# Kernel tuning notes

Measured on AMD Instinct MI355X. Metric: run time of the kernel, lower is better.

## Reference

```python
import jax, jax.numpy as jnp
import numpy as np
import math

B, L = 16, 100
NC = 80
STRIDES = (8.0, 16.0, 32.0)
ANCHORS = np.array([[10., 13.], [16., 30.], [33., 23.], [30., 61.], [62., 45.],
                    [59., 119.], [116., 90.], [156., 198.], [373., 326.]], np.float32)
ANCH_MASKS = ((0, 1, 2), (3, 4, 5), (6, 7, 8))
THRESH = 4.0          # gt_match_max_ratio
CIOU_RATIO = 1.0
W_BOX, W_OBJ, W_CLS = 0.05, 1.0, 0.58
OV = 0.5              # overlap in assign_targets_to_proposals


def _bce(x, z):
    # binary_cross_entropy_with_logits, elementwise
    return -(z * jax.nn.log_sigmoid(x) + (1.0 - z) * jax.nn.log_sigmoid(-x))


def _ciou_xywh(b1, b2, eps=1e-9):
    # b1, b2: [M,4] center-x, center-y, w, h  (matches _bbox_iou with x1y1x2y2=False, CIoU=True)
    b1x1, b1x2 = b1[:, 0] - b1[:, 2] / 2, b1[:, 0] + b1[:, 2] / 2
    b1y1, b1y2 = b1[:, 1] - b1[:, 3] / 2, b1[:, 1] + b1[:, 3] / 2
    b2x1, b2x2 = b2[:, 0] - b2[:, 2] / 2, b2[:, 0] + b2[:, 2] / 2
    b2y1, b2y2 = b2[:, 1] - b2[:, 3] / 2, b2[:, 1] + b2[:, 3] / 2
    inter = jnp.clip(jnp.minimum(b1x2, b2x2) - jnp.maximum(b1x1, b2x1), 0) * \
            jnp.clip(jnp.minimum(b1y2, b2y2) - jnp.maximum(b1y1, b2y1), 0)
    w1, h1 = b1x2 - b1x1, b1y2 - b1y1 + eps
    w2, h2 = b2x2 - b2x1, b2y2 - b2y1 + eps
    union = w1 * h1 + w2 * h2 - inter + eps
    iou = inter / union
    cw = jnp.maximum(b1x2, b2x2) - jnp.minimum(b1x1, b2x1)
    ch = jnp.maximum(b1y2, b2y2) - jnp.minimum(b1y1, b2y1)
    c2 = cw ** 2 + ch ** 2 + eps
    rho2 = ((b2x1 + b2x2 - b1x1 - b1x2) ** 2 + (b2y1 + b2y2 - b1y1 - b1y2) ** 2) / 4
    v = (4.0 / math.pi ** 2) * (jnp.arctan(w2 / h2) - jnp.arctan(w1 / h1)) ** 2
    alpha = jax.lax.stop_gradient(v / (1.0 + eps - iou + v))  # torch.no_grad()
    return iou - (rho2 / c2 + v * alpha)


def _yolo_loss(y_pred0, y_pred1, y_pred2, y_true):
    # valid GT rows: nlabel counts rows with positive sum; valid rows assumed contiguous at front
    nlabel = (y_true.sum(-1) > 0).sum(-1)                                # [B]
    valid = (jnp.arange(L)[None, :] < nlabel[:, None]).reshape(-1)       # [N]
    batch_ids = jnp.repeat(jnp.arange(B), L)                             # [N]
    flat = y_true.reshape(-1, 5)
    gt_labels = flat[:, 4].astype(jnp.int32)
    # convert x1,y1,w,h -> cx,cy,w,h
    gt_boxes = jnp.concatenate([flat[:, :2] + flat[:, 2:4] / 2, flat[:, 2:4]], axis=1)
    N = B * L
    offsets = jnp.array([[0, 0], [-OV, 0], [0, -OV], [OV, 0], [0, OV]], jnp.float32)
    loss_box = jnp.float32(0.0)
    loss_obj = jnp.float32(0.0)
    loss_cls = jnp.float32(0.0)
    for li, out in enumerate((y_pred0, y_pred1, y_pred2)):
        s = STRIDES[li]
        anch = jnp.asarray(ANCHORS[list(ANCH_MASKS[li])] / s)            # [3,2] grid units
        H, Wd = out.shape[2], out.shape[3]
        nch = 5 + NC
        p = out.reshape(B, -1, nch, H, Wd).transpose(0, 1, 3, 4, 2)      # [B,3,H,W,nch]
        sgb = gt_boxes / s                                               # [N,4]
        # size_matched_idx
        r = sgb[:, None, 2:4] / anch[None]                               # [N,3,2]
        maxr = jnp.maximum(r, 1.0 / r).max(-1)                           # [N,3]
        match = (maxr < THRESH) & valid[:, None]                         # [N,3]
        # assign_targets_to_proposals: 5 offset candidates per (gt, anchor)
        x, y = sgb[:, 0], sgb[:, 1]
        fx, fy = jnp.mod(x, 1.0), jnp.mod(y, 1.0)
        cond = jnp.stack([
            jnp.ones_like(x, bool),
            (x > 1) & (fx < OV),
            (y > 1) & (fy < OV),
            (x < Wd - 1) & (fx > 1 - OV),
            (y < H - 1) & (fy > 1 - OV),
        ], axis=1)                                                       # [N,5]
        coords = (sgb[:, None, :2] + offsets[None]).astype(jnp.int32)    # [N,5,2] (trunc like .long())
        cmask = (match[:, :, None] & cond[:, None, :]).reshape(-1)       # [N*3*5]
        bf = jnp.broadcast_to(batch_ids[:, None, None], (N, 3, 5)).reshape(-1)
        af = jnp.broadcast_to(jnp.arange(3)[None, :, None], (N, 3, 5)).reshape(-1)
        gf = jnp.broadcast_to(jnp.arange(N)[:, None, None], (N, 3, 5)).reshape(-1)
        gxy = jnp.broadcast_to(coords[:, None, :, :], (N, 3, 5, 2)).reshape(-1, 2)
        gx, gy = gxy[:, 0], gxy[:, 1]
        pred = p[bf, af, gy, gx]                                         # [M,nch] (OOB gathers clamped; masked out)
        pxy = jax.nn.sigmoid(pred[:, :2]) + gxy.astype(pred.dtype)
        pwh = jnp.exp(pred[:, 2:4]) * anch[af]
        pbox = jnp.concatenate([pxy, pwh], axis=1)
        ci = _ciou_xywh(pbox, sgb[gf])                                   # [M]
        cm = cmask.astype(pred.dtype)
        nval = cm.sum()
        denom = jnp.maximum(nval, 1.0)
        loss_box = loss_box + jnp.where(nval > 0, ((1.0 - ci) * cm).sum() / denom, 0.0)
        # objectness target scatter (invalid candidates dropped via OOB batch index)
        obj_val = CIOU_RATIO * jnp.clip(ci, 0) + (1.0 - CIOU_RATIO)
        bs = jnp.where(cmask, bf, B)
        gt_obj = jnp.zeros((B, 3, H, Wd), pred.dtype).at[bs, af, gy, gx].set(obj_val, mode='drop')
        if NC > 1:
            zhot = jax.nn.one_hot(gt_labels[gf], NC, dtype=pred.dtype)
            bce_c = _bce(pred[:, 5:], zhot)
            loss_cls = loss_cls + jnp.where(nval > 0, (bce_c * cm[:, None]).sum() / (denom * NC), 0.0)
        loss_obj = loss_obj + _bce(p[..., 4], gt_obj).mean()
    lb, lo, lc = W_BOX * loss_box, W_OBJ * loss_obj, W_CLS * loss_cls
    return lb + lo + lc, lb, lo, lc


def setup_inputs():
    rng = np.random.default_rng(0)
    k0, k1, k2 = jax.random.split(jax.random.key(0), 3)
    y_pred0 = jax.random.normal(k0, (B, 3 * (5 + NC), 80, 80), jnp.float32)
    y_pred1 = jax.random.normal(k1, (B, 3 * (5 + NC), 40, 40), jnp.float32)
    y_pred2 = jax.random.normal(k2, (B, 3 * (5 + NC), 20, 20), jnp.float32)
    yt = np.zeros((B, L, 5), np.float32)
    n_valid = 70  # valid labels contiguous at the front, rest zero-padded
    yt[:, :n_valid, 0] = rng.uniform(1.0, 560.0, (B, n_valid))
    yt[:, :n_valid, 1] = rng.uniform(1.0, 560.0, (B, n_valid))
    yt[:, :n_valid, 2] = rng.uniform(8.0, 80.0, (B, n_valid))
    yt[:, :n_valid, 3] = rng.uniform(8.0, 80.0, (B, n_valid))
    yt[:, :n_valid, 4] = rng.integers(0, NC, (B, n_valid)).astype(np.float32)
    return {"y_pred0": y_pred0, "y_pred1": y_pred1, "y_pred2": y_pred2, "y_true": jnp.asarray(yt)}


def reference(y_pred0, y_pred1, y_pred2, y_true):
    return _yolo_loss(y_pred0, y_pred1, y_pred2, y_true)
```

## Files before the change

### kernel.cpp

```cpp
#include <hip/hip_runtime.h>
#include <math.h>

#define BB 16
#define LL 100
#define NCLS 80
#define CPB 282
#define CAP 288
#define NBLK 256
#define NTHR 1024

__device__ __constant__ int   d_W[3]     = {80, 40, 20};
__device__ __constant__ int   d_HW[3]    = {6400, 1600, 400};
__device__ __constant__ float d_stride[3]= {8.f, 16.f, 32.f};
__device__ __constant__ int   d_gtoff[3] = {0, 307200, 384000};
__device__ __constant__ float d_anch[3][3][2] = {
  {{10.f,13.f},{16.f,30.f},{33.f,23.f}},
  {{30.f,61.f},{62.f,45.f},{59.f,119.f}},
  {{116.f,90.f},{156.f,198.f},{373.f,326.f}}};


__device__ __forceinline__ float softplusf(float t) {
  return fmaxf(t, 0.f) + log1pf(expf(-fabsf(t)));
}
__device__ __forceinline__ float sigmoidf_(float x) {
  return 1.f / (1.f + expf(-x));
}

__device__ __forceinline__ float ciou_(float px, float py, float pw, float ph,
                                       float gx, float gy, float gw, float gh) {
  const float eps = 1e-9f;
  float b1x1 = px - pw*0.5f, b1x2 = px + pw*0.5f;
  float b1y1 = py - ph*0.5f, b1y2 = py + ph*0.5f;
  float b2x1 = gx - gw*0.5f, b2x2 = gx + gw*0.5f;
  float b2y1 = gy - gh*0.5f, b2y2 = gy + gh*0.5f;
  float iw = fmaxf(fminf(b1x2,b2x2) - fmaxf(b1x1,b2x1), 0.f);
  float ih = fmaxf(fminf(b1y2,b2y2) - fmaxf(b1y1,b2y1), 0.f);
  float inter = iw*ih;
  float w1 = b1x2-b1x1, h1 = b1y2-b1y1 + eps;
  float w2 = b2x2-b2x1, h2 = b2y2-b2y1 + eps;
  float uni = w1*h1 + w2*h2 - inter + eps;
  float iou = inter/uni;
  float cw = fmaxf(b1x2,b2x2) - fminf(b1x1,b2x1);
  float ch = fmaxf(b1y2,b2y2) - fminf(b1y1,b2y1);
  float c2 = cw*cw + ch*ch + eps;
  float dx = b2x1+b2x2-b1x1-b1x2;
  float dy = b2y1+b2y2-b1y1-b1y2;
  float rho2 = (dx*dx + dy*dy)*0.25f;
  float at = atanf(w2/h2) - atanf(w1/h1);
  float v = (float)(4.0/(M_PI*M_PI)) * at*at;
  float alpha = v / (1.0f + eps - iou + v);
  return iou - (rho2/c2 + v*alpha);
}

__global__ __launch_bounds__(NTHR)
void k_main(const float* __restrict__ p0, const float* __restrict__ p1,
            const float* __restrict__ p2, const float* __restrict__ yt,
            float* __restrict__ acc, float* __restrict__ out)
{
  __shared__ int s_nl[2];
  __shared__ int s_cnt;
  __shared__ unsigned s_cand[CAP];
  __shared__ float s_acc[15];

  const int blk = blockIdx.x, tid = threadIdx.x;

  if (tid < 2)  s_nl[tid] = 0;
  if (tid == 2) s_cnt = 0;
  if (tid >= 4 && tid < 19) s_acc[tid-4] = 0.f;

  const int t0 = blk*CPB;
  const int b_lo = t0/4500;
  int b_hi = (t0 + CPB - 1)/4500; if (b_hi > BB-1) b_hi = BB-1;
  __syncthreads();

  if (tid < LL) {
    const float* row = yt + (size_t)(b_lo*LL + tid)*5;
    if (row[0]+row[1]+row[2]+row[3]+row[4] > 0.f) atomicAdd(&s_nl[0], 1);
  } else if (tid >= 128 && tid < 128+LL && b_hi != b_lo) {
    const float* row = yt + (size_t)(b_hi*LL + (tid-128))*5;
    if (row[0]+row[1]+row[2]+row[3]+row[4] > 0.f) atomicAdd(&s_nl[1], 1);
  }
  __syncthreads();

  if (tid < CPB) {
    int t = t0 + tid;
    if (t < BB*LL*45) {
      int b = t/4500; int rem = t - b*4500;
      int g_loc = rem/45; int rem2 = rem - g_loc*45;
      int lvl = rem2/15, ao = rem2 - lvl*15, a = ao/5, o = ao - a*5;
      const float* row = yt + (size_t)(b*LL + g_loc)*5;
      float s = d_stride[lvl];
      int W = d_W[lvl];
      float cx = (row[0] + row[2]*0.5f)/s;
      float cy = (row[1] + row[3]*0.5f)/s;
      float w = row[2]/s, h = row[3]/s;
      float aw = d_anch[lvl][a][0]/s, ah = d_anch[lvl][a][1]/s;
      float rw = w/aw, rh = h/ah;
      float maxr = fmaxf(fmaxf(rw,1.f/rw), fmaxf(rh,1.f/rh));
      int nl = (b == b_lo) ? s_nl[0] : s_nl[1];
      bool m = (g_loc < nl) && (maxr < 4.0f);
      float fx = cx - floorf(cx), fy = cy - floorf(cy);
      bool c;
      switch (o) {
        case 0: c = true; break;
        case 1: c = (cx > 1.f) && (fx < 0.5f); break;
        case 2: c = (cy > 1.f) && (fy < 0.5f); break;
        case 3: c = (cx < (float)(W-1)) && (fx > 0.5f); break;
        default:c = (cy < (float)(W-1)) && (fy > 0.5f); break;
      }
      if (m && c) {
        const float offx[5] = {0.f,-0.5f,0.f,0.5f,0.f};
        const float offy[5] = {0.f,0.f,-0.5f,0.f,0.5f};
        int gx = (int)(cx + offx[o]);
        int gy = (int)(cy + offy[o]);
        int g = b*LL + g_loc;
        unsigned pk = ((unsigned)lvl<<27) | ((unsigned)a<<25) | ((unsigned)g<<14)
                    | ((unsigned)gy<<7) | (unsigned)gx;
        int idx = atomicAdd(&s_cnt, 1);
        s_cand[idx] = pk;
      }
    }
  }

  {
    int gt = blk*NTHR + tid;
    if (gt < 100800) {
      int e0 = gt*4;
      int lvl = (e0 < 307200) ? 0 : (e0 < 384000 ? 1 : 2);
      int HW = d_HW[lvl];
      int idx = e0 - d_gtoff[lvl];
      int b = idx/(3*HW); int r2 = idx - b*3*HW; int a = r2/HW; int pos = r2 - a*HW;
      const float* pr = (lvl==0) ? p0 : (lvl==1) ? p1 : p2;
      const float4 x4 = *(const float4*)(pr + (size_t)((b*255 + a*85 + 4)*HW + pos));
      float sp = softplusf(x4.x) + softplusf(x4.y) + softplusf(x4.z) + softplusf(x4.w);
      atomicAdd(&s_acc[9+lvl], sp);
    }
  }
  __syncthreads();

  {
    int wave = tid >> 6, lane = tid & 63;
    int n = s_cnt;
    float a0=0,a1=0,a2=0, c0=0,c1=0,c2=0, n0=0,n1=0,n2=0, z0=0,z1=0,z2=0;
    for (int i = wave; i < n; i += 16) {
      unsigned pk = s_cand[i];
      int gx  = pk & 127;
      int gy  = (pk>>7) & 127;
      int g   = (pk>>14) & 2047;
      int a   = (pk>>25) & 3;
      int lvl = (pk>>27) & 3;
      int b = g / LL;
      float s = d_stride[lvl];
      int W = d_W[lvl], HW = d_HW[lvl];
      const float* pr = (lvl==0) ? p0 : (lvl==1) ? p1 : p2;
      const float* row = yt + (size_t)g*5;
      float cx = (row[0] + row[2]*0.5f)/s;
      float cy = (row[1] + row[3]*0.5f)/s;
      float w  = row[2]/s, h = row[3]/s;
      int label = (int)row[4];
      float aw = d_anch[lvl][a][0]/s, ah = d_anch[lvl][a][1]/s;

      const float* base = pr + (size_t)((b*255 + a*85)*HW + gy*W + gx);
      float xA = base[(size_t)lane*HW];
      float xB = (lane < 21) ? base[(size_t)(64+lane)*HW] : 0.f;
      float x0 = __shfl(xA,0), x1 = __shfl(xA,1), x2 = __shfl(xA,2), x3 = __shfl(xA,3);
      float xobj = __shfl(xA,4);

      float pxc = sigmoidf_(x0) + (float)gx;
      float pyc = sigmoidf_(x1) + (float)gy;
      float pw = expf(x2)*aw, ph = expf(x3)*ah;
      float ci = ciou_(pxc,pyc,pw,ph, cx,cy,w,h);

      float cls = 0.f;
      if (lane >= 5) { int cc = lane-5;  cls += (cc==label) ? softplusf(-xA) : softplusf(xA); }
      if (lane < 21) { int cc = 59+lane; cls += (cc==label) ? softplusf(-xB) : softplusf(xB); }
      for (int off = 1; off < 64; off <<= 1) cls += __shfl_xor(cls, off);

      float bx = 1.f - ci;
      float zx = fmaxf(ci, 0.f) * xobj;
      if      (lvl == 0) { a0 += bx; c0 += cls; n0 += 1.f; z0 += zx; }
      else if (lvl == 1) { a1 += bx; c1 += cls; n1 += 1.f; z1 += zx; }
      else               { a2 += bx; c2 += cls; n2 += 1.f; z2 += zx; }
    }
    if (lane == 0) {
      if (n0 != 0.f) { atomicAdd(&s_acc[0],a0); atomicAdd(&s_acc[3],c0);
                       atomicAdd(&s_acc[6],n0); atomicAdd(&s_acc[12],z0); }
      if (n1 != 0.f) { atomicAdd(&s_acc[1],a1); atomicAdd(&s_acc[4],c1);
                       atomicAdd(&s_acc[7],n1); atomicAdd(&s_acc[13],z1); }
      if (n2 != 0.f) { atomicAdd(&s_acc[2],a2); atomicAdd(&s_acc[5],c2);
                       atomicAdd(&s_acc[8],n2); atomicAdd(&s_acc[14],z2); }
    }
  }
  __syncthreads();
  if (tid < 15 && s_acc[tid] != 0.f) atomicAdd(&acc[tid], s_acc[tid]);
  __syncthreads();

  if (tid == 0) {
    __threadfence();
    unsigned old = atomicAdd((unsigned int*)&acc[15], 1u);
    if (old == (unsigned)(gridDim.x - 1)) {
      float A[15];
      #pragma unroll
      for (int k = 0; k < 15; ++k) A[k] = atomicAdd(&acc[k], 0.0f);
      const float cells[3] = {307200.f, 76800.f, 19200.f};
      float lb = 0.f, lc = 0.f, lo = 0.f;
      for (int l = 0; l < 3; ++l) {
        float nval  = A[6+l];
        float denom = fmaxf(nval, 1.f);
        if (nval > 0.f) {
          lb += A[l] / denom;
          lc += A[3+l] / (denom * (float)NCLS);
        }
        lo += (A[9+l] - A[12+l]) / cells[l];
      }
      lb *= 0.05f;
      lc *= 0.58f;
      out[0] = lb + lo + lc;
      out[1] = lb;
      out[2] = lo;
      out[3] = lc;
    }
  }
}

extern "C" void kernel_launch(void* const* d_in, const int* in_sizes, int n_in,
                              void* d_out, int out_size, void* d_ws, size_t ws_size,
                              hipStream_t stream) {
  const float* p0 = (const float*)d_in[0];
  const float* p1 = (const float*)d_in[1];
  const float* p2 = (const float*)d_in[2];
  const float* yt = (const float*)d_in[3];
  float* acc = (float*)d_ws;

  hipMemsetAsync(acc, 0, 16*sizeof(float), stream);
  k_main<<<NBLK, NTHR, 0, stream>>>(p0, p1, p2, yt, acc, (float*)d_out);
}
```

Before: 55.47 us.

## Split fused loss kernel into prep, wide gather, and finalize kernels

Splits the single fused kernel into three launches. Candidate generation writes its packed candidates to global workspace, and a second kernel assigns one wave per candidate slot across 4608 blocks plus 99 blocks for the objectness softplus sum. A tiny final kernel replaces the last-block atomic-counter finalization and the memset. The aim is to spread the serial per-block candidate loop across far more waves, at the cost of two extra launches and many blocks that find no candidate in their slot.

```diff
diff --git a/kernel.cpp b/kernel.cpp
--- a/kernel.cpp
+++ b/kernel.cpp
@@ -6,7 +6,9 @@
 #define NCLS 80
 #define CPB 282
 #define CAP 288
-#define NBLK 256
+#define PREPB 256
+#define GATB 4608
+#define OBJB 99
 #define NTHR 1024
 
 __device__ __constant__ int   d_W[3]     = {80, 40, 20};
@@ -18,6 +20,9 @@
   {{30.f,61.f},{62.f,45.f},{59.f,119.f}},
   {{116.f,90.f},{156.f,198.f},{373.f,326.f}}};
 
+#define ACC_OFF   0
+#define CNT_OFF   16
+#define CANDG_OFF 272
 
 __device__ __forceinline__ float softplusf(float t) {
   return fmaxf(t, 0.f) + log1pf(expf(-fabsf(t)));
@@ -52,21 +57,18 @@
   return iou - (rho2/c2 + v*alpha);
 }
 
-__global__ __launch_bounds__(NTHR)
-void k_main(const float* __restrict__ p0, const float* __restrict__ p1,
-            const float* __restrict__ p2, const float* __restrict__ yt,
-            float* __restrict__ acc, float* __restrict__ out)
+__global__ __launch_bounds__(512)
+void k_prep(const float* __restrict__ yt, float* __restrict__ acc,
+            unsigned int* __restrict__ cntg, unsigned int* __restrict__ candg)
 {
   __shared__ int s_nl[2];
   __shared__ int s_cnt;
-  __shared__ unsigned s_cand[CAP];
-  __shared__ float s_acc[15];
-
   const int blk = blockIdx.x, tid = threadIdx.x;
+
+  if (blk == 0 && tid >= 32 && tid < 48) acc[tid-32] = 0.f;
 
   if (tid < 2)  s_nl[tid] = 0;
   if (tid == 2) s_cnt = 0;
-  if (tid >= 4 && tid < 19) s_acc[tid-4] = 0.f;
 
   const int t0 = blk*CPB;
   const int b_lo = t0/4500;
@@ -117,33 +119,33 @@
         unsigned pk = ((unsigned)lvl<<27) | ((unsigned)a<<25) | ((unsigned)g<<14)
                     | ((unsigned)gy<<7) | (unsigned)gx;
         int idx = atomicAdd(&s_cnt, 1);
-        s_cand[idx] = pk;
+        candg[blk*CAP + idx] = pk;
       }
     }
   }
-
-  {
-    int gt = blk*NTHR + tid;
-    if (gt < 100800) {
-      int e0 = gt*4;
-      int lvl = (e0 < 307200) ? 0 : (e0 < 384000 ? 1 : 2);
-      int HW = d_HW[lvl];
-      int idx = e0 - d_gtoff[lvl];
-      int b = idx/(3*HW); int r2 = idx - b*3*HW; int a = r2/HW; int pos = r2 - a*HW;
-      const float* pr = (lvl==0) ? p0 : (lvl==1) ? p1 : p2;
-      const float4 x4 = *(const float4*)(pr + (size_t)((b*255 + a*85 + 4)*HW + pos));
-      float sp = softplusf(x4.x) + softplusf(x4.y) + softplusf(x4.z) + softplusf(x4.w);
-      atomicAdd(&s_acc[9+lvl], sp);
-    }
-  }
-  __syncthreads();
-
-  {
-    int wave = tid >> 6, lane = tid & 63;
-    int n = s_cnt;
-    float a0=0,a1=0,a2=0, c0=0,c1=0,c2=0, n0=0,n1=0,n2=0, z0=0,z1=0,z2=0;
-    for (int i = wave; i < n; i += 16) {
-      unsigned pk = s_cand[i];
+  __syncthreads();
+  if (tid == 0) cntg[blk] = (unsigned)s_cnt;
+}
+
+__global__ __launch_bounds__(NTHR)
+void k_gather(const float* __restrict__ p0, const float* __restrict__ p1,
+              const float* __restrict__ p2, const float* __restrict__ yt,
+              const unsigned int* __restrict__ cntg,
+              const unsigned int* __restrict__ candg,
+              float* __restrict__ acc)
+{
+  __shared__ float s_acc[15];
+  const int blk = blockIdx.x, tid = threadIdx.x;
+  if (tid < 15) s_acc[tid] = 0.f;
+  __syncthreads();
+
+  if (blk < GATB) {
+    int wg = blk*16 + (tid >> 6);
+    int lane = tid & 63;
+    int p = wg / CAP;
+    int sIdx = wg - p*CAP;
+    if (sIdx < (int)cntg[p]) {
+      unsigned pk = candg[p*CAP + sIdx];
       int gx  = pk & 127;
       int gy  = (pk>>7) & 127;
       int g   = (pk>>14) & 2047;
@@ -176,51 +178,53 @@
       if (lane < 21) { int cc = 59+lane; cls += (cc==label) ? softplusf(-xB) : softplusf(xB); }
       for (int off = 1; off < 64; off <<= 1) cls += __shfl_xor(cls, off);
 
-      float bx = 1.f - ci;
-      float zx = fmaxf(ci, 0.f) * xobj;
-      if      (lvl == 0) { a0 += bx; c0 += cls; n0 += 1.f; z0 += zx; }
-      else if (lvl == 1) { a1 += bx; c1 += cls; n1 += 1.f; z1 += zx; }
-      else               { a2 += bx; c2 += cls; n2 += 1.f; z2 += zx; }
-    }
-    if (lane == 0) {
-      if (n0 != 0.f) { atomicAdd(&s_acc[0],a0); atomicAdd(&s_acc[3],c0);
-                       atomicAdd(&s_acc[6],n0); atomicAdd(&s_acc[12],z0); }
-      if (n1 != 0.f) { atomicAdd(&s_acc[1],a1); atomicAdd(&s_acc[4],c1);
-                       atomicAdd(&s_acc[7],n1); atomicAdd(&s_acc[13],z1); }
-      if (n2 != 0.f) { atomicAdd(&s_acc[2],a2); atomicAdd(&s_acc[5],c2);
-                       atomicAdd(&s_acc[8],n2); atomicAdd(&s_acc[14],z2); }
+      if (lane == 0) {
+        float bx = 1.f - ci;
+        float zx = fmaxf(ci, 0.f) * xobj;
+        atomicAdd(&s_acc[lvl],     bx);
+        atomicAdd(&s_acc[3+lvl],  cls);
+        atomicAdd(&s_acc[6+lvl],  1.f);
+        atomicAdd(&s_acc[12+lvl], zx);
+      }
+    }
+  } else {
+    int gt = (blk - GATB)*NTHR + tid;
+    if (gt < 100800) {
+      int e0 = gt*4;
+      int lvl = (e0 < 307200) ? 0 : (e0 < 384000 ? 1 : 2);
+      int HW = d_HW[lvl];
+      int idx = e0 - d_gtoff[lvl];
+      int b = idx/(3*HW); int r2 = idx - b*3*HW; int a = r2/HW; int pos = r2 - a*HW;
+      const float* pr = (lvl==0) ? p0 : (lvl==1) ? p1 : p2;
+      const float4 x4 = *(const float4*)(pr + (size_t)((b*255 + a*85 + 4)*HW + pos));
+      float sp = softplusf(x4.x) + softplusf(x4.y) + softplusf(x4.z) + softplusf(x4.w);
+      atomicAdd(&s_acc[9+lvl], sp);
     }
   }
   __syncthreads();
   if (tid < 15 && s_acc[tid] != 0.f) atomicAdd(&acc[tid], s_acc[tid]);
-  __syncthreads();
-
-  if (tid == 0) {
-    __threadfence();
-    unsigned old = atomicAdd((unsigned int*)&acc[15], 1u);
-    if (old == (unsigned)(gridDim.x - 1)) {
-      float A[15];
-      #pragma unroll
-      for (int k = 0; k < 15; ++k) A[k] = atomicAdd(&acc[k], 0.0f);
-      const float cells[3] = {307200.f, 76800.f, 19200.f};
-      float lb = 0.f, lc = 0.f, lo = 0.f;
-      for (int l = 0; l < 3; ++l) {
-        float nval  = A[6+l];
-        float denom = fmaxf(nval, 1.f);
-        if (nval > 0.f) {
-          lb += A[l] / denom;
-          lc += A[3+l] / (denom * (float)NCLS);
-        }
-        lo += (A[9+l] - A[12+l]) / cells[l];
-      }
-      lb *= 0.05f;
-      lc *= 0.58f;
-      out[0] = lb + lo + lc;
-      out[1] = lb;
-      out[2] = lo;
-      out[3] = lc;
-    }
-  }
+}
+
+__global__ __launch_bounds__(64)
+void k_fin(const float* __restrict__ acc, float* __restrict__ out) {
+  if (threadIdx.x != 0) return;
+  const float cells[3] = {307200.f, 76800.f, 19200.f};
+  float lb = 0.f, lc = 0.f, lo = 0.f;
+  for (int l = 0; l < 3; ++l) {
+    float nval  = acc[6+l];
+    float denom = fmaxf(nval, 1.f);
+    if (nval > 0.f) {
+      lb += acc[l] / denom;
+      lc += acc[3+l] / (denom * (float)NCLS);
+    }
+    lo += (acc[9+l] - acc[12+l]) / cells[l];
+  }
+  lb *= 0.05f;
+  lc *= 0.58f;
+  out[0] = lb + lo + lc;
+  out[1] = lb;
+  out[2] = lo;
+  out[3] = lc;
 }
 
 extern "C" void kernel_launch(void* const* d_in, const int* in_sizes, int n_in,
@@ -230,8 +234,13 @@
   const float* p1 = (const float*)d_in[1];
   const float* p2 = (const float*)d_in[2];
   const float* yt = (const float*)d_in[3];
-  float* acc = (float*)d_ws;
-
-  hipMemsetAsync(acc, 0, 16*sizeof(float), stream);
-  k_main<<<NBLK, NTHR, 0, stream>>>(p0, p1, p2, yt, acc, (float*)d_out);
-}
+
+  float*        wsf   = (float*)d_ws;
+  float*        acc   = wsf + ACC_OFF;
+  unsigned int* cntg  = (unsigned int*)(wsf + CNT_OFF);
+  unsigned int* candg = (unsigned int*)(wsf + CANDG_OFF);
+
+  k_prep  <<<PREPB, 512, 0, stream>>>(yt, acc, cntg, candg);
+  k_gather<<<GATB + OBJB, NTHR, 0, stream>>>(p0, p1, p2, yt, cntg, candg, acc);
+  k_fin   <<<1, 64, 0, stream>>>(acc, (float*)d_out);
+}
```

Result: faster. 47.71 us (-14.0%).

## Split loss kernel into prep, compaction and wide gather stages

Applied to the files above, without the earlier changes.

The single fused kernel is split into three launches. The first builds candidate matches per block into global memory. A single-block prefix scan then compacts them into one list. A wide gather kernel spreads candidates across many more waves, roughly one per wave, while dedicated blocks handle the objectness softplus sum. The aim is to remove the long serial per-block candidate loop, at the cost of two extra launches and a serial copy loop in the compaction kernel.

```diff
diff --git a/kernel.cpp b/kernel.cpp
--- a/kernel.cpp
+++ b/kernel.cpp
@@ -6,7 +6,9 @@
 #define NCLS 80
 #define CPB 282
 #define CAP 288
-#define NBLK 256
+#define PREPB 256
+#define OBJB 99
+#define GATB 1024
 #define NTHR 1024
 
 __device__ __constant__ int   d_W[3]     = {80, 40, 20};
@@ -18,6 +20,11 @@
   {{30.f,61.f},{62.f,45.f},{59.f,119.f}},
   {{116.f,90.f},{156.f,198.f},{373.f,326.f}}};
 
+#define ACC_OFF    0
+#define CNT_OFF    16
+#define CANDG_OFF  272
+#define PACK_OFF   74000
+#define NCAND_OFF  146000
 
 __device__ __forceinline__ float softplusf(float t) {
   return fmaxf(t, 0.f) + log1pf(expf(-fabsf(t)));
@@ -52,21 +59,18 @@
   return iou - (rho2/c2 + v*alpha);
 }
 
-__global__ __launch_bounds__(NTHR)
-void k_main(const float* __restrict__ p0, const float* __restrict__ p1,
-            const float* __restrict__ p2, const float* __restrict__ yt,
-            float* __restrict__ acc, float* __restrict__ out)
+__global__ __launch_bounds__(512)
+void k_prep(const float* __restrict__ yt, float* __restrict__ acc,
+            unsigned int* __restrict__ cntg, unsigned int* __restrict__ candg)
 {
   __shared__ int s_nl[2];
   __shared__ int s_cnt;
-  __shared__ unsigned s_cand[CAP];
-  __shared__ float s_acc[15];
-
   const int blk = blockIdx.x, tid = threadIdx.x;
+
+  if (blk == 0 && tid >= 32 && tid < 48) acc[tid-32] = 0.f;
 
   if (tid < 2)  s_nl[tid] = 0;
   if (tid == 2) s_cnt = 0;
-  if (tid >= 4 && tid < 19) s_acc[tid-4] = 0.f;
 
   const int t0 = blk*CPB;
   const int b_lo = t0/4500;
@@ -117,33 +121,70 @@
         unsigned pk = ((unsigned)lvl<<27) | ((unsigned)a<<25) | ((unsigned)g<<14)
                     | ((unsigned)gy<<7) | (unsigned)gx;
         int idx = atomicAdd(&s_cnt, 1);
-        s_cand[idx] = pk;
-      }
-    }
-  }
-
-  {
+        candg[blk*CAP + idx] = pk;
+      }
+    }
+  }
+  __syncthreads();
+  if (tid == 0) cntg[blk] = (unsigned)s_cnt;
+}
+
+__global__ __launch_bounds__(256)
+void k_compact(const unsigned int* __restrict__ cntg,
+               const unsigned int* __restrict__ candg,
+               unsigned int* __restrict__ packed,
+               unsigned int* __restrict__ ncand)
+{
+  __shared__ unsigned s[256];
+  const int t = threadIdx.x;
+  unsigned cnt = cntg[t];
+  s[t] = cnt;
+  __syncthreads();
+  for (int off = 1; off < 256; off <<= 1) {
+    unsigned v = (t >= off) ? s[t-off] : 0u;
+    __syncthreads();
+    s[t] += v;
+    __syncthreads();
+  }
+  unsigned base = s[t] - cnt;
+  for (unsigned i = 0; i < cnt; ++i)
+    packed[base + i] = candg[t*CAP + i];
+  if (t == 255) *ncand = s[255];
+}
+
+__global__ __launch_bounds__(NTHR)
+void k_gather(const float* __restrict__ p0, const float* __restrict__ p1,
+              const float* __restrict__ p2, const float* __restrict__ yt,
+              const unsigned int* __restrict__ ncand,
+              const unsigned int* __restrict__ packed,
+              float* __restrict__ acc, float* __restrict__ out)
+{
+  __shared__ float s_acc[15];
+  const int blk = blockIdx.x, tid = threadIdx.x;
+  if (tid < 15) s_acc[tid] = 0.f;
+  __syncthreads();
+
+  if (blk < OBJB) {
     int gt = blk*NTHR + tid;
+    float so = 0.f; int lvl = 0;
     if (gt < 100800) {
       int e0 = gt*4;
-      int lvl = (e0 < 307200) ? 0 : (e0 < 384000 ? 1 : 2);
+      lvl = (e0 < 307200) ? 0 : (e0 < 384000 ? 1 : 2);
       int HW = d_HW[lvl];
       int idx = e0 - d_gtoff[lvl];
       int b = idx/(3*HW); int r2 = idx - b*3*HW; int a = r2/HW; int pos = r2 - a*HW;
       const float* pr = (lvl==0) ? p0 : (lvl==1) ? p1 : p2;
-      const float4 x4 = *(const float4*)(pr + (size_t)((b*255 + a*85 + 4)*HW + pos));
-      float sp = softplusf(x4.x) + softplusf(x4.y) + softplusf(x4.z) + softplusf(x4.w);
-      atomicAdd(&s_acc[9+lvl], sp);
-    }
-  }
-  __syncthreads();
-
-  {
-    int wave = tid >> 6, lane = tid & 63;
-    int n = s_cnt;
-    float a0=0,a1=0,a2=0, c0=0,c1=0,c2=0, n0=0,n1=0,n2=0, z0=0,z1=0,z2=0;
-    for (int i = wave; i < n; i += 16) {
-      unsigned pk = s_cand[i];
+      const float4 o4 = *(const float4*)(pr + (size_t)((b*255 + a*85 + 4)*HW + pos));
+      so = softplusf(o4.x) + softplusf(o4.y) + softplusf(o4.z) + softplusf(o4.w);
+    }
+    for (int off = 1; off < 64; off <<= 1) so += __shfl_xor(so, off);
+    if ((tid & 63) == 0 && so != 0.f) atomicAdd(&s_acc[9+lvl], so);
+  } else {
+    const int nc = (int)*ncand;
+    const int wv = (blk - OBJB)*16 + (tid >> 6);
+    const int lane = tid & 63;
+    for (int i = wv; i < nc; i += GATB*16) {
+      unsigned pk = packed[i];
       int gx  = pk & 127;
       int gy  = (pk>>7) & 127;
       int g   = (pk>>14) & 2047;
@@ -176,19 +217,14 @@
       if (lane < 21) { int cc = 59+lane; cls += (cc==label) ? softplusf(-xB) : softplusf(xB); }
       for (int off = 1; off < 64; off <<= 1) cls += __shfl_xor(cls, off);
 
-      float bx = 1.f - ci;
-      float zx = fmaxf(ci, 0.f) * xobj;
-      if      (lvl == 0) { a0 += bx; c0 += cls; n0 += 1.f; z0 += zx; }
-      else if (lvl == 1) { a1 += bx; c1 += cls; n1 += 1.f; z1 += zx; }
-      else               { a2 += bx; c2 += cls; n2 += 1.f; z2 += zx; }
-    }
-    if (lane == 0) {
-      if (n0 != 0.f) { atomicAdd(&s_acc[0],a0); atomicAdd(&s_acc[3],c0);
-                       atomicAdd(&s_acc[6],n0); atomicAdd(&s_acc[12],z0); }
-      if (n1 != 0.f) { atomicAdd(&s_acc[1],a1); atomicAdd(&s_acc[4],c1);
-                       atomicAdd(&s_acc[7],n1); atomicAdd(&s_acc[13],z1); }
-      if (n2 != 0.f) { atomicAdd(&s_acc[2],a2); atomicAdd(&s_acc[5],c2);
-                       atomicAdd(&s_acc[8],n2); atomicAdd(&s_acc[14],z2); }
+      if (lane == 0) {
+        float bx = 1.f - ci;
+        float zx = fmaxf(ci, 0.f) * xobj;
+        atomicAdd(&s_acc[lvl],     bx);
+        atomicAdd(&s_acc[3+lvl],  cls);
+        atomicAdd(&s_acc[6+lvl],  1.f);
+        atomicAdd(&s_acc[12+lvl], zx);
+      }
     }
   }
   __syncthreads();
@@ -230,8 +266,16 @@
   const float* p1 = (const float*)d_in[1];
   const float* p2 = (const float*)d_in[2];
   const float* yt = (const float*)d_in[3];
-  float* acc = (float*)d_ws;
-
-  hipMemsetAsync(acc, 0, 16*sizeof(float), stream);
-  k_main<<<NBLK, NTHR, 0, stream>>>(p0, p1, p2, yt, acc, (float*)d_out);
-}
+
+  float*        wsf    = (float*)d_ws;
+  float*        acc    = wsf + ACC_OFF;
+  unsigned int* cntg   = (unsigned int*)(wsf + CNT_OFF);
+  unsigned int* candg  = (unsigned int*)(wsf + CANDG_OFF);
+  unsigned int* packed = (unsigned int*)(wsf + PACK_OFF);
+  unsigned int* ncand  = (unsigned int*)(wsf + NCAND_OFF);
+
+  k_prep   <<<PREPB, 512, 0, stream>>>(yt, acc, cntg, candg);
+  k_compact<<<1, 256, 0, stream>>>(cntg, candg, packed, ncand);
+  k_gather <<<OBJB + GATB, NTHR, 0, stream>>>(p0, p1, p2, yt, ncand, packed,
+                                              acc, (float*)d_out);
+}
```

Result: slower. 80.95 us (+45.9%).
